# Kernel tuning notes

Measured on AMD Instinct MI355X. Metric: run time of the kernel, lower is better.

The kernel has to match this reference:

```python
import jax, jax.numpy as jnp
import numpy as np

EMBED_LEN = 512
NUM_FEA = 8   # M
NUM_CLS = 14  # C
BETA = 0.3
BATCH = 8192


def setup_inputs() -> dict:
    key = jax.random.key(0)
    k1, k2, k3 = jax.random.split(key, 3)
    x = jax.random.normal(k1, (BATCH, EMBED_LEN * NUM_FEA), dtype=jnp.float32)
    wordvec_array = jax.random.normal(k2, (1, EMBED_LEN, NUM_CLS), dtype=jnp.float32)
    y = jax.random.randint(k3, (BATCH, NUM_CLS), 0, 2, dtype=jnp.int32)
    # guarantee at least one positive and one negative label per sample
    y = y.at[:, 0].set(1).at[:, -1].set(0)
    return {"x": x, "y": y, "wordvec_array": wordvec_array}


def reference(x, y, wordvec_array):
    B = x.shape[0]
    un = x.reshape(B, EMBED_LEN, -1)            # [B, E, M]
    w = wordvec_array[0]                         # [E, C]
    # dot_prod_all[b, c] = max_m <un[b,:,m], w[:,c]>
    dot = jnp.einsum('bem,ec->bmc', un, w).max(axis=1)   # [B, C]

    P = (y == 1).astype(x.dtype)                 # positive mask [B, C]
    N = 1.0 - P                                  # negative mask [B, C]
    npos = P.sum(axis=-1)                        # [B]
    nneg = N.sum(axis=-1)                        # [B]

    # pairwise v[b,p,n] = dot_neg - dot_pos; sum softplus over masked pairs
    V = dot[:, None, :] - dot[:, :, None]        # [B, C(pos), C(neg)]
    pair_sum = jnp.einsum('bp,bn,bpn->b', P, N, jax.nn.softplus(V))
    # edge case: no negatives -> v = -dot_pos
    noneg_sum = jnp.sum(P * jax.nn.softplus(-dot), axis=-1)
    S = jnp.where(nneg > 0, pair_sum, noneg_sum)
    base = S / npos                              # [B]

    # diversity: unbiased variance of positive-class word vectors over class dim
    mean_w = jnp.einsum('bc,ec->be', P, w) / npos[:, None]          # [B, E]
    ss = jnp.einsum('bc,bec->be', P, (w[None] - mean_w[:, :, None]) ** 2)
    var_w = ss / jnp.maximum(npos - 1.0, 1.0)[:, None]
    var_w = jnp.where((npos == 1.0)[:, None], 0.0, var_w)           # sig = 0 if single positive
    total_var = var_w.sum(axis=-1)               # [B]

    # var_regularization: unbiased var over M, L1 over embed dim
    sig2 = jnp.var(un, axis=2, ddof=1)           # [B, E]
    l1_err = jnp.abs(sig2).sum(axis=-1)          # [B]

    # num_fea > 1 branch
    loss = 2.0 * ((1.0 - BETA) * (1.0 + total_var) * base + BETA * l1_err)
    return loss.mean()
```

## Files before the change

kernel.cpp:

```cpp
#include <hip/hip_runtime.h>
#include <math.h>

#define E_LEN 512
#define C_CLS 14
#define BATCH 8192
#define S_PER_BLOCK 4
#define NSLOTS 256
#define SCR_STRIDE 68

typedef float v2f __attribute__((ext_vector_type(2)));
typedef float v4f __attribute__((ext_vector_type(4)));

#define PK_FMA_LO(acc, u, wv) \
  asm("v_pk_fma_f32 %0, %1, %2, %0 op_sel_hi:[1,0,1]" : "+v"(acc) : "v"(u), "v"(wv))
#define PK_FMA_HI(acc, u, wv) \
  asm("v_pk_fma_f32 %0, %1, %2, %0 op_sel:[0,1,0]" : "+v"(acc) : "v"(u), "v"(wv))
#define PK_MUL_LO(d, u, wv) \
  asm("v_pk_mul_f32 %0, %1, %2 op_sel_hi:[1,0]" : "=v"(d) : "v"(u), "v"(wv))
#define PK_MUL_HI(d, u, wv) \
  asm("v_pk_mul_f32 %0, %1, %2 op_sel:[0,1]" : "=v"(d) : "v"(u), "v"(wv))

#define BAR() asm volatile("s_waitcnt lgkmcnt(0)\ns_barrier" ::: "memory")

template<int CTRL>
__device__ __forceinline__ float dpp_mov_f(float v) {
  return __int_as_float(__builtin_amdgcn_update_dpp(
      0, __float_as_int(v), CTRL, 0xF, 0xF, false));
}
__device__ __forceinline__ float sum16(float v) {
  v += dpp_mov_f<0x128>(v);
  v += dpp_mov_f<0x124>(v);
  v += dpp_mov_f<0x122>(v);
  v += dpp_mov_f<0x121>(v);
  return v;
}
__device__ __forceinline__ float wsum64(float v) {
  v = sum16(v);
  v += dpp_mov_f<0x142>(v);
  v += dpp_mov_f<0x143>(v);
  return v;
}
__device__ __forceinline__ float rl63(float v) {
  return __int_as_float(__builtin_amdgcn_readlane(__float_as_int(v), 63));
}
__device__ __forceinline__ float max8(float v) {
  v = fmaxf(v, dpp_mov_f<0xB1>(v));
  v = fmaxf(v, dpp_mov_f<0x4E>(v));
  v = fmaxf(v, dpp_mov_f<0x141>(v));
  return v;
}
__device__ __forceinline__ float softplus_f(float v) {
  return fmaxf(v, 0.f) + __logf(1.f + __expf(-fabsf(v)));
}

__global__ void MID_LOSS_prep(const float* __restrict__ w,
                              float* __restrict__ wsf) {
  __shared__ float wl[E_LEN * C_CLS];
  const int tid = threadIdx.x;
#pragma unroll
  for (int i = 0; i < 7; ++i)
    ((float4*)wl)[tid + i * 256] = ((const float4*)w)[tid + i * 256];
  wsf[tid] = 0.f;
  __syncthreads();
  if (tid < 196) {
    const int p = tid / 14, n = tid - p * 14;
    float g = 0.f;
    for (int e = 0; e < E_LEN; ++e)
      g = fmaf(wl[e * 14 + p], wl[e * 14 + n], g);
    wsf[NSLOTS + tid] = g;
  }
}

__global__ __launch_bounds__(256, 4)
void MID_LOSS_main(const float* __restrict__ x, const int* __restrict__ y,
                   const float* __restrict__ w, const float* __restrict__ wsf,
                   float* __restrict__ slots) {
  __shared__ alignas(16) float wp_s[7 * 1024];
  __shared__ alignas(16) float scr[14 * SCR_STRIDE];
  __shared__ alignas(8)  float var_s[E_LEN * 2];
  __shared__ float G_s[196];
  __shared__ float P4_s[S_PER_BLOCK * C_CLS];
  __shared__ float dot_s[C_CLS];
  __shared__ float l1_scr[8];
  __shared__ float npos_s[S_PER_BLOCK];
  __shared__ float w2sum_s[S_PER_BLOCK];

  const int tid = threadIdx.x;
  const int lane = tid & 63;
  const int wid = tid >> 6;
  const int mh = wid & 1;
  const int eh = wid >> 1;
  const int ebase = eh * 256 + lane;
  const int b0 = blockIdx.x * S_PER_BLOCK;

  alignas(16) v2f U[2][4][2];
  {
    const float* xr = x + (size_t)b0 * (E_LEN * 8);
#pragma unroll
    for (int j = 0; j < 4; ++j)
      *(v4f*)&U[0][j][0] = *(const v4f*)(xr + (ebase + j * 64) * 8 + mh * 4);
  }

#pragma unroll
  for (int i = 0; i < 7; ++i) {
    const int idx = tid + i * 256;
    const v4f v = ((const v4f*)w)[idx];
#pragma unroll
    for (int k = 0; k < 4; ++k) {
      const int f = idx * 4 + k;
      const int e = f / 14;
      const int c = f - e * 14;
      wp_s[(c >> 1) * 1024 + e * 2 + (c & 1)] = v[k];
    }
  }
  if (tid < 196) G_s[tid] = wsf[NSLOTS + tid];
  if (tid < S_PER_BLOCK * C_CLS)
    P4_s[tid] = (y[b0 * C_CLS + tid] == 1) ? 1.f : 0.f;
  BAR();
  if (tid < S_PER_BLOCK) {
    float np = 0.f;
    for (int c = 0; c < C_CLS; ++c) np += P4_s[tid * C_CLS + c];
    npos_s[tid] = np;
  } else if (tid < 2 * S_PER_BLOCK) {
    const int s = tid - S_PER_BLOCK;
    float sw = 0.f;
    for (int c = 0; c < C_CLS; ++c)
      sw = fmaf(P4_s[s * C_CLS + c], G_s[c * 15], sw);
    w2sum_s[s] = sw;
  }
  BAR();

  float block_loss = 0.f;

#pragma unroll
  for (int s = 0; s < S_PER_BLOCK; ++s) {
    const int cur = s & 1, nxt = cur ^ 1;

    float vs1[4], vs2[4];
#pragma unroll
    for (int j = 0; j < 4; ++j) {
      const v2f t = U[cur][j][0] + U[cur][j][1];
      vs1[j] = t.x + t.y;
      v2f q = U[cur][j][0] * U[cur][j][0];
      q += U[cur][j][1] * U[cur][j][1];
      vs2[j] = q.x + q.y;
    }
    if (mh == 1) {
#pragma unroll
      for (int j = 0; j < 4; ++j) {
        v2f o;
        o.x = vs1[j];
        o.y = vs2[j];
        *(v2f*)(var_s + 2 * (ebase + j * 64)) = o;
      }
    }

    alignas(16) v2f acc[14][2];
#pragma unroll
    for (int j = 0; j < 4; ++j) {
      const int e = ebase + j * 64;
      const float* wb = wp_s + e * 2;
#pragma unroll
      for (int cp = 0; cp < 7; ++cp) {
        const v2f wv = *(const v2f*)(wb + cp * 1024);
        if (j == 0) {
          PK_MUL_LO(acc[2 * cp][0], U[cur][0][0], wv);
          PK_MUL_LO(acc[2 * cp][1], U[cur][0][1], wv);
          PK_MUL_HI(acc[2 * cp + 1][0], U[cur][0][0], wv);
          PK_MUL_HI(acc[2 * cp + 1][1], U[cur][0][1], wv);
        } else {
          PK_FMA_LO(acc[2 * cp][0], U[cur][j][0], wv);
          PK_FMA_LO(acc[2 * cp][1], U[cur][j][1], wv);
          PK_FMA_HI(acc[2 * cp + 1][0], U[cur][j][0], wv);
          PK_FMA_HI(acc[2 * cp + 1][1], U[cur][j][1], wv);
        }
      }
    }

    if (s < S_PER_BLOCK - 1) {
      const float* xn = x + (size_t)(b0 + s + 1) * (E_LEN * 8);
#pragma unroll
      for (int j = 0; j < 4; ++j)
        *(v4f*)&U[nxt][j][0] = *(const v4f*)(xn + (ebase + j * 64) * 8 + mh * 4);
    }

#pragma unroll
    for (int c = 0; c < 14; ++c) {
      acc[c][0].x = sum16(acc[c][0].x);
      acc[c][0].y = sum16(acc[c][0].y);
      acc[c][1].x = sum16(acc[c][1].x);
      acc[c][1].y = sum16(acc[c][1].y);
    }
    if ((lane & 15) == 0) {
      float* sp = scr + (eh * 4 + (lane >> 4)) * 8 + mh * 4;
#pragma unroll
      for (int c = 0; c < 14; ++c)
        *(float4*)(sp + c * SCR_STRIDE) = *(float4*)&acc[c][0];
    }
    BAR();

    if (mh == 1) {
      const int r = eh * 64 + lane;
      const int craw = r >> 3;
      const int c = (craw > 13) ? 13 : craw;
      const int m = r & 7;
      const float* sp = scr + c * SCR_STRIDE + m;
      float dv = sp[0] + sp[8] + sp[16] + sp[24] + sp[32] + sp[40] + sp[48] + sp[56];
      dv = max8(dv);
      if ((r & 7) == 0 && craw < 14) dot_s[c] = dv;
    } else {
      float l1 = 0.f;
#pragma unroll
      for (int j = 0; j < 4; ++j) {
        const v2f o = *(const v2f*)(var_s + 2 * (ebase + j * 64));
        const float s1 = vs1[j] + o.x;
        const float s2 = vs2[j] + o.y;
        const float sig = (s2 - s1 * s1 * 0.125f) * (1.f / 7.f);
        l1 += fabsf(sig);
      }
      l1 = sum16(l1);
      if ((lane & 15) == 0) l1_scr[eh * 4 + (lane >> 4)] = l1;
    }
    BAR();

    if (wid == 0) {
      const float* Pv = P4_s + s * C_CLS;
      float Sc = 0.f, Gc = 0.f, Lc = 0.f;
#pragma unroll
      for (int k = 0; k < 4; ++k) {
        const int tt = lane + k * 64;
        if (tt < 196) {
          const int p = (tt * 2341) >> 15;
          const int n = tt - p * 14;
          const float Pp = Pv[p], Pn = Pv[n];
          Sc += Pp * (1.f - Pn) * softplus_f(dot_s[n] - dot_s[p]);
          Gc = fmaf(Pp * Pn, G_s[tt], Gc);
        }
      }
      if (lane < 8) Lc = l1_scr[lane];
      Sc = wsum64(Sc);
      Gc = wsum64(Gc);
      Lc = wsum64(Lc);
      const float S = rl63(Sc), sumG = rl63(Gc), l1e = rl63(Lc);
      const float npos = npos_s[s];
      const float base = S / npos;
      const float tv =
          (npos > 1.5f) ? (w2sum_s[s] - sumG / npos) / (npos - 1.f) : 0.f;
      block_loss += 1.4f * (1.f + tv) * base + 0.6f * l1e;
    }
  }
  if (tid == 0) atomicAdd(&slots[blockIdx.x & (NSLOTS - 1)], block_loss);
}

__global__ void MID_LOSS_fin(const float* __restrict__ wsf,
                             float* __restrict__ out) {
  const int tid = threadIdx.x;
  float s = wsf[tid] + wsf[tid + 64] + wsf[tid + 128] + wsf[tid + 192];
  s = wsum64(s);
  if (tid == 63) out[0] = s * (1.f / (float)BATCH);
}

extern "C" void kernel_launch(void* const* d_in, const int* in_sizes, int n_in,
                              void* d_out, int out_size, void* d_ws, size_t ws_size,
                              hipStream_t stream) {
  const float* x = (const float*)d_in[0];
  const int* y = (const int*)d_in[1];
  const float* w = (const float*)d_in[2];
  float* out = (float*)d_out;
  float* wsf = (float*)d_ws;

  MID_LOSS_prep<<<1, 256, 0, stream>>>(w, wsf);
  MID_LOSS_main<<<BATCH / S_PER_BLOCK, 256, 0, stream>>>(x, y, w, wsf, wsf);
  MID_LOSS_fin<<<1, 64, 0, stream>>>(wsf, out);
}
```

Before: 256.5 us.

## Rewrite main kernel around bf16 MFMA for dot products and variance

After: 216.8 us. 15.5% less time.

```diff
diff --git a/kernel.cpp b/kernel.cpp
--- a/kernel.cpp
+++ b/kernel.cpp
@@ -4,23 +4,17 @@
 #define E_LEN 512
 #define C_CLS 14
 #define BATCH 8192
-#define S_PER_BLOCK 4
 #define NSLOTS 256
-#define SCR_STRIDE 68
-
-typedef float v2f __attribute__((ext_vector_type(2)));
+#define WS_G 256
+#define WS_WB 464
+#define WB_ROW 260
+
 typedef float v4f __attribute__((ext_vector_type(4)));
-
-#define PK_FMA_LO(acc, u, wv) \
-  asm("v_pk_fma_f32 %0, %1, %2, %0 op_sel_hi:[1,0,1]" : "+v"(acc) : "v"(u), "v"(wv))
-#define PK_FMA_HI(acc, u, wv) \
-  asm("v_pk_fma_f32 %0, %1, %2, %0 op_sel:[0,1,0]" : "+v"(acc) : "v"(u), "v"(wv))
-#define PK_MUL_LO(d, u, wv) \
-  asm("v_pk_mul_f32 %0, %1, %2 op_sel_hi:[1,0]" : "=v"(d) : "v"(u), "v"(wv))
-#define PK_MUL_HI(d, u, wv) \
-  asm("v_pk_mul_f32 %0, %1, %2 op_sel:[0,1]" : "=v"(d) : "v"(u), "v"(wv))
-
-#define BAR() asm volatile("s_waitcnt lgkmcnt(0)\ns_barrier" ::: "memory")
+typedef short s8v __attribute__((ext_vector_type(8)));
+union APk { int i[4]; s8v s; };
+
+#define CVT_PK_BF16(d, a, b) \
+  asm("v_cvt_pk_bf16_f32 %0, %1, %2" : "=v"(d) : "v"(a), "v"(b))
 
 template<int CTRL>
 __device__ __forceinline__ float dpp_mov_f(float v) {
@@ -34,20 +28,23 @@
   v += dpp_mov_f<0x121>(v);
   return v;
 }
+__device__ __forceinline__ float hsum32(float v) {
+  v = sum16(v);
+  v += dpp_mov_f<0x142>(v);
+  return v;
+}
 __device__ __forceinline__ float wsum64(float v) {
   v = sum16(v);
   v += dpp_mov_f<0x142>(v);
   v += dpp_mov_f<0x143>(v);
   return v;
 }
-__device__ __forceinline__ float rl63(float v) {
-  return __int_as_float(__builtin_amdgcn_readlane(__float_as_int(v), 63));
-}
-__device__ __forceinline__ float max8(float v) {
-  v = fmaxf(v, dpp_mov_f<0xB1>(v));
-  v = fmaxf(v, dpp_mov_f<0x4E>(v));
-  v = fmaxf(v, dpp_mov_f<0x141>(v));
-  return v;
+template<int PAT>
+__device__ __forceinline__ float swz_f(float v) {
+  return __int_as_float(__builtin_amdgcn_ds_swizzle(__float_as_int(v), PAT));
+}
+__device__ __forceinline__ float shfl_x32(float v) {
+  return __shfl_xor(v, 32, 64);
 }
 __device__ __forceinline__ float softplus_f(float v) {
   return fmaxf(v, 0.f) + __logf(1.f + __expf(-fabsf(v)));
@@ -67,189 +64,120 @@
     float g = 0.f;
     for (int e = 0; e < E_LEN; ++e)
       g = fmaf(wl[e * 14 + p], wl[e * 14 + n], g);
-    wsf[NSLOTS + tid] = g;
+    wsf[WS_G + tid] = g;
+  }
+  unsigned int* wsu = (unsigned int*)wsf;
+  for (int i = tid; i < 4096; i += 256) {
+    const int c = i >> 8;
+    const int ep = i & 255;
+    const int e = ep * 2;
+    const float v0 = (c < 14) ? wl[e * 14 + c] : 0.f;
+    const float v1 = (c < 14) ? wl[(e + 1) * 14 + c] : 0.f;
+    int d;
+    CVT_PK_BF16(d, v0, v1);
+    wsu[WS_WB + c * WB_ROW + ep] = (unsigned int)d;
   }
 }
 
 __global__ __launch_bounds__(256, 4)
 void MID_LOSS_main(const float* __restrict__ x, const int* __restrict__ y,
-                   const float* __restrict__ w, const float* __restrict__ wsf,
-                   float* __restrict__ slots) {
-  __shared__ alignas(16) float wp_s[7 * 1024];
-  __shared__ alignas(16) float scr[14 * SCR_STRIDE];
-  __shared__ alignas(8)  float var_s[E_LEN * 2];
-  __shared__ float G_s[196];
-  __shared__ float P4_s[S_PER_BLOCK * C_CLS];
-  __shared__ float dot_s[C_CLS];
-  __shared__ float l1_scr[8];
-  __shared__ float npos_s[S_PER_BLOCK];
-  __shared__ float w2sum_s[S_PER_BLOCK];
+                   const float* __restrict__ wsf, float* __restrict__ slots) {
+  __shared__ unsigned int wB_l[16 * WB_ROW];
+  __shared__ float G_l[196];
+  __shared__ float dots_l[4][2][16];
+  __shared__ float P_l[4][2][16];
 
   const int tid = threadIdx.x;
   const int lane = tid & 63;
   const int wid = tid >> 6;
-  const int mh = wid & 1;
-  const int eh = wid >> 1;
-  const int ebase = eh * 256 + lane;
-  const int b0 = blockIdx.x * S_PER_BLOCK;
-
-  alignas(16) v2f U[2][4][2];
-  {
-    const float* xr = x + (size_t)b0 * (E_LEN * 8);
-#pragma unroll
-    for (int j = 0; j < 4; ++j)
-      *(v4f*)&U[0][j][0] = *(const v4f*)(xr + (ebase + j * 64) * 8 + mh * 4);
-  }
-
-#pragma unroll
-  for (int i = 0; i < 7; ++i) {
-    const int idx = tid + i * 256;
-    const v4f v = ((const v4f*)w)[idx];
-#pragma unroll
-    for (int k = 0; k < 4; ++k) {
-      const int f = idx * 4 + k;
-      const int e = f / 14;
-      const int c = f - e * 14;
-      wp_s[(c >> 1) * 1024 + e * 2 + (c & 1)] = v[k];
+  const unsigned int* wsu = (const unsigned int*)wsf;
+
+  for (int i = tid; i < 16 * WB_ROW; i += 256) wB_l[i] = wsu[WS_WB + i];
+  if (tid < 196) G_l[tid] = wsf[WS_G + tid];
+  __syncthreads();
+
+  const int row = lane & 15;
+  const int kg = lane >> 4;
+  const int b0 = blockIdx.x * 8 + wid * 2;
+  const int b = b0 + (row >> 3);
+  const int m = row & 7;
+  const float* xp = x + (size_t)b * (E_LEN * 8) + kg * 64 + m;
+
+  v4f acc = {0.f, 0.f, 0.f, 0.f};
+  v4f acc2 = {0.f, 0.f, 0.f, 0.f};
+  float q = 0.f;
+#pragma unroll
+  for (int ch = 0; ch < 16; ++ch) {
+    const float* xc = xp + ch * 256;
+    float u[8];
+#pragma unroll
+    for (int j = 0; j < 8; ++j) u[j] = xc[j * 8];
+#pragma unroll
+    for (int j = 0; j < 8; ++j) q = fmaf(u[j], u[j], q);
+    APk a;
+#pragma unroll
+    for (int jj = 0; jj < 4; ++jj) CVT_PK_BF16(a.i[jj], u[2 * jj], u[2 * jj + 1]);
+    const s8v bfrag =
+        *(const s8v*)(wB_l + (lane & 15) * WB_ROW + ch * 16 + kg * 4);
+    acc = __builtin_amdgcn_mfma_f32_16x16x32_bf16(a.s, bfrag, acc, 0, 0, 0);
+    acc2 = __builtin_amdgcn_mfma_f32_16x16x32_bf16(a.s, a.s, acc2, 0, 0, 0);
+  }
+
+  if (lane < 28) {
+    const int s = (lane >= 14) ? 1 : 0;
+    P_l[wid][s][lane - s * 14] = (y[b0 * 14 + lane] == 1) ? 1.f : 0.f;
+  }
+
+  float dmax = fmaxf(fmaxf(acc[0], acc[1]), fmaxf(acc[2], acc[3]));
+  dmax = fmaxf(dmax, swz_f<0x401F>(dmax));
+  if ((lane & 16) == 0 && (lane & 15) < 14)
+    dots_l[wid][lane >> 5][lane & 15] = dmax;
+
+  const float loc2 = acc2[0] + acc2[1] + acc2[2] + acc2[3];
+  const bool validb = (((lane & 15) < 8) == (lane < 32));
+  float s2v = validb ? loc2 : 0.f;
+  float q2 = q + shfl_x32(q);
+  float qv = validb ? q2 : 0.f;
+
+  asm volatile("s_waitcnt lgkmcnt(0)" ::: "memory");
+
+  const int half = lane >> 5;
+  const int hl = lane & 31;
+  const float* dp = dots_l[wid][half];
+  const float* Pp = P_l[wid][half];
+  float S = 0.f, Gc = 0.f;
+#pragma unroll
+  for (int r = 0; r < 7; ++r) {
+    const int tt = r * 28 + hl;
+    if (hl < 28) {
+      const int p = (tt * 2341) >> 15;
+      const int n = tt - p * 14;
+      const float Ppv = Pp[p], Pnv = Pp[n];
+      S += Ppv * (1.f - Pnv) * softplus_f(dp[n] - dp[p]);
+      Gc = fmaf(Ppv * Pnv, G_l[tt], Gc);
     }
   }
-  if (tid < 196) G_s[tid] = wsf[NSLOTS + tid];
-  if (tid < S_PER_BLOCK * C_CLS)
-    P4_s[tid] = (y[b0 * C_CLS + tid] == 1) ? 1.f : 0.f;
-  BAR();
-  if (tid < S_PER_BLOCK) {
-    float np = 0.f;
-    for (int c = 0; c < C_CLS; ++c) np += P4_s[tid * C_CLS + c];
-    npos_s[tid] = np;
-  } else if (tid < 2 * S_PER_BLOCK) {
-    const int s = tid - S_PER_BLOCK;
-    float sw = 0.f;
-    for (int c = 0; c < C_CLS; ++c)
-      sw = fmaf(P4_s[s * C_CLS + c], G_s[c * 15], sw);
-    w2sum_s[s] = sw;
-  }
-  BAR();
-
-  float block_loss = 0.f;
-
-#pragma unroll
-  for (int s = 0; s < S_PER_BLOCK; ++s) {
-    const int cur = s & 1, nxt = cur ^ 1;
-
-    float vs1[4], vs2[4];
-#pragma unroll
-    for (int j = 0; j < 4; ++j) {
-      const v2f t = U[cur][j][0] + U[cur][j][1];
-      vs1[j] = t.x + t.y;
-      v2f q = U[cur][j][0] * U[cur][j][0];
-      q += U[cur][j][1] * U[cur][j][1];
-      vs2[j] = q.x + q.y;
-    }
-    if (mh == 1) {
-#pragma unroll
-      for (int j = 0; j < 4; ++j) {
-        v2f o;
-        o.x = vs1[j];
-        o.y = vs2[j];
-        *(v2f*)(var_s + 2 * (ebase + j * 64)) = o;
-      }
-    }
-
-    alignas(16) v2f acc[14][2];
-#pragma unroll
-    for (int j = 0; j < 4; ++j) {
-      const int e = ebase + j * 64;
-      const float* wb = wp_s + e * 2;
-#pragma unroll
-      for (int cp = 0; cp < 7; ++cp) {
-        const v2f wv = *(const v2f*)(wb + cp * 1024);
-        if (j == 0) {
-          PK_MUL_LO(acc[2 * cp][0], U[cur][0][0], wv);
-          PK_MUL_LO(acc[2 * cp][1], U[cur][0][1], wv);
-          PK_MUL_HI(acc[2 * cp + 1][0], U[cur][0][0], wv);
-          PK_MUL_HI(acc[2 * cp + 1][1], U[cur][0][1], wv);
-        } else {
-          PK_FMA_LO(acc[2 * cp][0], U[cur][j][0], wv);
-          PK_FMA_LO(acc[2 * cp][1], U[cur][j][1], wv);
-          PK_FMA_HI(acc[2 * cp + 1][0], U[cur][j][0], wv);
-          PK_FMA_HI(acc[2 * cp + 1][1], U[cur][j][1], wv);
-        }
-      }
-    }
-
-    if (s < S_PER_BLOCK - 1) {
-      const float* xn = x + (size_t)(b0 + s + 1) * (E_LEN * 8);
-#pragma unroll
-      for (int j = 0; j < 4; ++j)
-        *(v4f*)&U[nxt][j][0] = *(const v4f*)(xn + (ebase + j * 64) * 8 + mh * 4);
-    }
-
-#pragma unroll
-    for (int c = 0; c < 14; ++c) {
-      acc[c][0].x = sum16(acc[c][0].x);
-      acc[c][0].y = sum16(acc[c][0].y);
-      acc[c][1].x = sum16(acc[c][1].x);
-      acc[c][1].y = sum16(acc[c][1].y);
-    }
-    if ((lane & 15) == 0) {
-      float* sp = scr + (eh * 4 + (lane >> 4)) * 8 + mh * 4;
-#pragma unroll
-      for (int c = 0; c < 14; ++c)
-        *(float4*)(sp + c * SCR_STRIDE) = *(float4*)&acc[c][0];
-    }
-    BAR();
-
-    if (mh == 1) {
-      const int r = eh * 64 + lane;
-      const int craw = r >> 3;
-      const int c = (craw > 13) ? 13 : craw;
-      const int m = r & 7;
-      const float* sp = scr + c * SCR_STRIDE + m;
-      float dv = sp[0] + sp[8] + sp[16] + sp[24] + sp[32] + sp[40] + sp[48] + sp[56];
-      dv = max8(dv);
-      if ((r & 7) == 0 && craw < 14) dot_s[c] = dv;
-    } else {
-      float l1 = 0.f;
-#pragma unroll
-      for (int j = 0; j < 4; ++j) {
-        const v2f o = *(const v2f*)(var_s + 2 * (ebase + j * 64));
-        const float s1 = vs1[j] + o.x;
-        const float s2 = vs2[j] + o.y;
-        const float sig = (s2 - s1 * s1 * 0.125f) * (1.f / 7.f);
-        l1 += fabsf(sig);
-      }
-      l1 = sum16(l1);
-      if ((lane & 15) == 0) l1_scr[eh * 4 + (lane >> 4)] = l1;
-    }
-    BAR();
-
-    if (wid == 0) {
-      const float* Pv = P4_s + s * C_CLS;
-      float Sc = 0.f, Gc = 0.f, Lc = 0.f;
-#pragma unroll
-      for (int k = 0; k < 4; ++k) {
-        const int tt = lane + k * 64;
-        if (tt < 196) {
-          const int p = (tt * 2341) >> 15;
-          const int n = tt - p * 14;
-          const float Pp = Pv[p], Pn = Pv[n];
-          Sc += Pp * (1.f - Pn) * softplus_f(dot_s[n] - dot_s[p]);
-          Gc = fmaf(Pp * Pn, G_s[tt], Gc);
-        }
-      }
-      if (lane < 8) Lc = l1_scr[lane];
-      Sc = wsum64(Sc);
-      Gc = wsum64(Gc);
-      Lc = wsum64(Lc);
-      const float S = rl63(Sc), sumG = rl63(Gc), l1e = rl63(Lc);
-      const float npos = npos_s[s];
-      const float base = S / npos;
-      const float tv =
-          (npos > 1.5f) ? (w2sum_s[s] - sumG / npos) / (npos - 1.f) : 0.f;
-      block_loss += 1.4f * (1.f + tv) * base + 0.6f * l1e;
-    }
-  }
-  if (tid == 0) atomicAdd(&slots[blockIdx.x & (NSLOTS - 1)], block_loss);
+  float npv = (hl < 14) ? Pp[hl] : 0.f;
+  float w2v = (hl < 14) ? Pp[hl] * G_l[hl * 15] : 0.f;
+
+  S = hsum32(S);
+  Gc = hsum32(Gc);
+  s2v = hsum32(s2v);
+  qv = hsum32(qv);
+  npv = hsum32(npv);
+  w2v = hsum32(w2v);
+
+  float loss = 0.f;
+  if ((lane & 31) == 31) {
+    const float npos = npv;
+    const float base = S / npos;
+    const float tv =
+        (npos > 1.5f) ? (w2v - Gc / npos) / (npos - 1.f) : 0.f;
+    const float l1 = (qv - s2v * 0.125f) * (1.f / 7.f);
+    loss = 1.4f * (1.f + tv) * base + 0.6f * l1;
+  }
+  loss += shfl_x32(loss);
+  if (lane == 31) atomicAdd(&slots[blockIdx.x & (NSLOTS - 1)], loss);
 }
 
 __global__ void MID_LOSS_fin(const float* __restrict__ wsf,
@@ -270,6 +198,6 @@
   float* wsf = (float*)d_ws;
 
   MID_LOSS_prep<<<1, 256, 0, stream>>>(w, wsf);
-  MID_LOSS_main<<<BATCH / S_PER_BLOCK, 256, 0, stream>>>(x, y, w, wsf, wsf);
+  MID_LOSS_main<<<BATCH / 8, 256, 0, stream>>>(x, y, wsf, wsf);
   MID_LOSS_fin<<<1, 64, 0, stream>>>(wsf, out);
 }
```
